# Performance work log

Measured on AMD Instinct MI355X. Metric: run time of the kernel, lower is better.

Reference implementation:

```python
import jax, jax.numpy as jnp
import numpy as np
from jax.scipy.linalg import solve_triangular

D = 1792  # feature dim, divisible by m=28
B = 8192  # batch (columns of X)


def setup_inputs() -> dict:
    key = jax.random.key(0)
    k1, k2 = jax.random.split(key)
    X = jax.random.normal(k1, (D, B), dtype=jnp.float32)
    # matches torch.zeros((d,d)).normal_(0, 0.05)
    U = jax.random.normal(k2, (D, D), dtype=jnp.float32) * 0.05
    return {"X": X, "U": U}


def reference(X, U):
    """Product of d Householder reflections applied to X.

    Original math (sequential_mult): for row = d-1..0:
        X <- X - 2 v_row (v_row^T X),  v_row = U[row] / ||U[row]||
    i.e. X <- H_0 H_1 ... H_{d-1} X with H_i = I - 2 v_i v_i^T.

    We use the compact WY representation instead of the sequential loop:
        P = H_0 ... H_{d-1} = I - W^T V_n
    where rows w_k of W satisfy w_k = 2 v_k - 2 sum_{j<k} (v_j . v_k) w_j,
    i.e. (I + 2 * strict_tril(G)) W = 2 V_n with G = V_n V_n^T.
    This is the same math, expressed with GEMMs + one triangular solve.
    """
    Vn = U / jnp.linalg.norm(U, axis=1, keepdims=True)          # (d, d) unit reflector rows
    G = Vn @ Vn.T                                               # (d, d) gram of reflectors
    T = jnp.eye(D, dtype=X.dtype) + 2.0 * jnp.tril(G, k=-1)    # unit-diag lower triangular
    Wt = solve_triangular(T, 2.0 * Vn, lower=True)              # (d, d): rows are w_k
    return X - Wt.T @ (Vn @ X)                                  # P @ X
```

## Files before the change

kernel.cpp:

```cpp
#include <hip/hip_runtime.h>
#include <stdint.h>
#include <stddef.h>

typedef _Float16 half_t;
typedef _Float16 half8 __attribute__((ext_vector_type(8)));
typedef float float4v __attribute__((ext_vector_type(4)));

#define D_DIM 1792
#define B_DIM 8192

__device__ __forceinline__ void stage_rows(const half_t* __restrict__ src, int row0, int ld,
                                           int k0, half_t* dst, int nchunks, int tid) {
  for (int base = 0; base < nchunks; base += 256) {
    int ch  = base + tid;
    int row = ch >> 2, kc = ch & 3;
    int swz = kc ^ ((row >> 1) & 3);
    const half_t* g = src + (size_t)(row0 + row) * ld + k0 + swz * 8;
    half_t* l = dst + (size_t)(base + (tid & 192)) * 8;
    __builtin_amdgcn_global_load_lds(
        (const __attribute__((address_space(1))) uint32_t*)(const void*)g,
        (__attribute__((address_space(3))) uint32_t*)(void*)l, 16, 0, 0);
  }
}

__device__ __forceinline__ void stage_rows64(const half_t* __restrict__ src, int row0, int ld,
                                             int k0, half_t* dst, int nchunks, int tid) {
  for (int base = 0; base < nchunks; base += 256) {
    int ch  = base + tid;
    int row = ch >> 3, kc = ch & 7;
    int swz = kc ^ (row & 7);
    const half_t* g = src + (size_t)(row0 + row) * ld + k0 + swz * 8;
    half_t* l = dst + (size_t)(base + (tid & 192)) * 8;
    __builtin_amdgcn_global_load_lds(
        (const __attribute__((address_space(1))) uint32_t*)(const void*)g,
        (__attribute__((address_space(3))) uint32_t*)(void*)l, 16, 0, 0);
  }
}

__device__ __forceinline__ half8 frag32(const half_t* lds, int row, int chunk) {
  int slot = chunk ^ ((row >> 1) & 3);
  return *(const half8*)(lds + row * 32 + slot * 8);
}
__device__ __forceinline__ half8 frag64(const half_t* lds, int row, int chunk) {
  int slot = chunk ^ (row & 7);
  return *(const half8*)(lds + row * 64 + slot * 8);
}

__global__ __launch_bounds__(256) void normalize_rows(const float* __restrict__ U,
                                                      half_t* __restrict__ Vh) {
  int r = blockIdx.x, t = threadIdx.x;
  float v[7];
  float s = 0.f;
#pragma unroll
  for (int i = 0; i < 7; ++i) {
    v[i] = U[(size_t)r * D_DIM + t + i * 256];
    s += v[i] * v[i];
  }
#pragma unroll
  for (int m = 32; m; m >>= 1) s += __shfl_xor(s, m);
  __shared__ float red[4];
  __shared__ float tot;
  if ((t & 63) == 0) red[t >> 6] = s;
  __syncthreads();
  if (t == 0) tot = 1.0f / sqrtf(red[0] + red[1] + red[2] + red[3]);
  __syncthreads();
  float rn = tot;
#pragma unroll
  for (int i = 0; i < 7; ++i)
    Vh[(size_t)r * D_DIM + t + i * 256] = (half_t)(v[i] * rn);
}

__global__ __launch_bounds__(256) void transpose_x(const float* __restrict__ X,
                                                   half_t* __restrict__ XT) {
  __shared__ half_t t[64][68];
  int r0 = blockIdx.x * 64, c0 = blockIdx.y * 64;
  int tid = threadIdx.x;
#pragma unroll
  for (int i = 0; i < 16; ++i) {
    int f = tid + i * 256;
    int rr = f >> 6, cc = f & 63;
    t[rr][cc] = (half_t)X[(size_t)(r0 + rr) * B_DIM + c0 + cc];
  }
  __syncthreads();
#pragma unroll
  for (int i = 0; i < 16; ++i) {
    int f = tid + i * 256;
    int cc = f >> 6, rr = f & 63;
    XT[(size_t)(c0 + cc) * D_DIM + r0 + rr] = t[rr][cc];
  }
}

__global__ __launch_bounds__(256) void transpose_h(const half_t* __restrict__ Vh,
                                                   half_t* __restrict__ VhT) {
  __shared__ half_t t[64][68];
  int r0 = blockIdx.x * 64, c0 = blockIdx.y * 64;
  int tid = threadIdx.x;
#pragma unroll
  for (int i = 0; i < 16; ++i) {
    int f = tid + i * 256;
    int rr = f >> 6, cc = f & 63;
    t[rr][cc] = Vh[(size_t)(r0 + rr) * D_DIM + c0 + cc];
  }
  __syncthreads();
#pragma unroll
  for (int i = 0; i < 16; ++i) {
    int f = tid + i * 256;
    int cc = f >> 6, rr = f & 63;
    VhT[(size_t)(c0 + cc) * D_DIM + r0 + rr] = t[rr][cc];
  }
}

__global__ __launch_bounds__(256) void zero_tri(half_t* __restrict__ Tinv,
                                                half_t* __restrict__ TinvT) {
  int bc = blockIdx.x, br = blockIdx.y;
  int tid = threadIdx.x;
  half8 z = {};
  if (bc > br) {
    for (int it = 0; it < 8; ++it) {
      int ch = it * 256 + tid;
      int r = ch >> 4, c = (ch & 15) * 8;
      *(half8*)(Tinv + (size_t)(br * 128 + r) * D_DIM + bc * 128 + c) = z;
    }
  } else if (bc < br) {
    for (int it = 0; it < 8; ++it) {
      int ch = it * 256 + tid;
      int r = ch >> 4, c = (ch & 15) * 8;
      *(half8*)(TinvT + (size_t)(br * 128 + r) * D_DIM + bc * 128 + c) = z;
    }
  }
}

template <int MODE>
__global__ __launch_bounds__(256) void gemm_nt(const half_t* __restrict__ A,
                                               const half_t* __restrict__ B,
                                               float* __restrict__ Cf, half_t* __restrict__ Ch,
                                               int K, int lda, int ldb, int ldc) {
  int bx = blockIdx.x, by = blockIdx.y;
  if constexpr (MODE == 2) {
    int id = bx + gridDim.x * by;
    int xcd = id & 7, s = id >> 3;
    by = s % 14;
    bx = (s / 14) * 8 + xcd;
  }
  int m0 = by * 128, n0 = bx * 128;
  __shared__ half_t sA0[128 * 32], sB0[128 * 32];
  __shared__ half_t sA1[128 * 32], sB1[128 * 32];
  int tid = threadIdx.x, lane = tid & 63, wave = tid >> 6;
  int ln15 = lane & 15, quad = lane >> 4;
  int wr = (wave & 1) * 64, wc = (wave >> 1) * 64;
  float4v acc[4][4] = {};
  int KB = K / 32;
  auto compute = [&](const half_t* cA, const half_t* cB) {
    half8 af[4], bf[4];
#pragma unroll
    for (int i = 0; i < 4; ++i) af[i] = frag32(cA, wr + i * 16 + ln15, quad);
#pragma unroll
    for (int j = 0; j < 4; ++j) bf[j] = frag32(cB, wc + j * 16 + ln15, quad);
#pragma unroll
    for (int i = 0; i < 4; ++i)
#pragma unroll
      for (int j = 0; j < 4; ++j)
        acc[i][j] = __builtin_amdgcn_mfma_f32_16x16x32_f16(af[i], bf[j], acc[i][j], 0, 0, 0);
  };
  stage_rows(A, m0, lda, 0, sA0, 512, tid);
  stage_rows(B, n0, ldb, 0, sB0, 512, tid);
  for (int kb = 0; kb < KB; kb += 2) {
    stage_rows(A, m0, lda, (kb + 1) * 32, sA1, 512, tid);
    stage_rows(B, n0, ldb, (kb + 1) * 32, sB1, 512, tid);
    asm volatile("s_waitcnt vmcnt(4)" ::: "memory");
    __builtin_amdgcn_s_barrier();
    __builtin_amdgcn_sched_barrier(0);
    compute(sA0, sB0);
    __builtin_amdgcn_sched_barrier(0);
    __builtin_amdgcn_s_barrier();
    if (kb + 2 < KB) {
      stage_rows(A, m0, lda, (kb + 2) * 32, sA0, 512, tid);
      stage_rows(B, n0, ldb, (kb + 2) * 32, sB0, 512, tid);
      asm volatile("s_waitcnt vmcnt(4)" ::: "memory");
    } else {
      asm volatile("s_waitcnt vmcnt(0)" ::: "memory");
    }
    __builtin_amdgcn_s_barrier();
    __builtin_amdgcn_sched_barrier(0);
    compute(sA1, sB1);
    __builtin_amdgcn_sched_barrier(0);
    __builtin_amdgcn_s_barrier();
  }
#pragma unroll
  for (int i = 0; i < 4; ++i)
#pragma unroll
    for (int j = 0; j < 4; ++j)
#pragma unroll
      for (int rg = 0; rg < 4; ++rg) {
        int row = m0 + wr + i * 16 + quad * 4 + rg;
        int col = n0 + wc + j * 16 + ln15;
        Cf[(size_t)row * ldc + col] = acc[i][j][rg];
      }
}

template <int MODE>
__global__ __launch_bounds__(256) void gemm64(const half_t* __restrict__ A,
                                              const half_t* __restrict__ B,
                                              half_t* __restrict__ Ch,
                                              int K, int lda, int ldb, int ldc) {
  int m0 = blockIdx.y * 64, n0 = blockIdx.x * 64;
  if constexpr (MODE == 0) { if (n0 > m0) return; }
  int Keff = K;
  if constexpr (MODE == 3) Keff = n0 + 64;
  __shared__ half_t sA0[64 * 32], sB0[64 * 32];
  __shared__ half_t sA1[64 * 32], sB1[64 * 32];
  int tid = threadIdx.x, lane = tid & 63, wave = tid >> 6;
  int ln15 = lane & 15, quad = lane >> 4;
  int wr = (wave & 1) * 32, wc = (wave >> 1) * 32;
  float4v acc[2][2] = {};
  int KB = Keff / 32;
  auto compute = [&](const half_t* cA, const half_t* cB) {
    half8 af[2], bf[2];
#pragma unroll
    for (int i = 0; i < 2; ++i) af[i] = frag32(cA, wr + i * 16 + ln15, quad);
#pragma unroll
    for (int j = 0; j < 2; ++j) bf[j] = frag32(cB, wc + j * 16 + ln15, quad);
#pragma unroll
    for (int i = 0; i < 2; ++i)
#pragma unroll
      for (int j = 0; j < 2; ++j)
        acc[i][j] = __builtin_amdgcn_mfma_f32_16x16x32_f16(af[i], bf[j], acc[i][j], 0, 0, 0);
  };
  stage_rows(A, m0, lda, 0, sA0, 256, tid);
  stage_rows(B, n0, ldb, 0, sB0, 256, tid);
  for (int kb = 0; kb < KB; kb += 2) {
    stage_rows(A, m0, lda, (kb + 1) * 32, sA1, 256, tid);
    stage_rows(B, n0, ldb, (kb + 1) * 32, sB1, 256, tid);
    asm volatile("s_waitcnt vmcnt(2)" ::: "memory");
    __builtin_amdgcn_s_barrier();
    __builtin_amdgcn_sched_barrier(0);
    compute(sA0, sB0);
    __builtin_amdgcn_sched_barrier(0);
    __builtin_amdgcn_s_barrier();
    if (kb + 2 < KB) {
      stage_rows(A, m0, lda, (kb + 2) * 32, sA0, 256, tid);
      stage_rows(B, n0, ldb, (kb + 2) * 32, sB0, 256, tid);
      asm volatile("s_waitcnt vmcnt(2)" ::: "memory");
    } else {
      asm volatile("s_waitcnt vmcnt(0)" ::: "memory");
    }
    __builtin_amdgcn_s_barrier();
    __builtin_amdgcn_sched_barrier(0);
    compute(sA1, sB1);
    __builtin_amdgcn_sched_barrier(0);
    __builtin_amdgcn_s_barrier();
  }
#pragma unroll
  for (int i = 0; i < 2; ++i)
#pragma unroll
    for (int j = 0; j < 2; ++j)
#pragma unroll
      for (int rg = 0; rg < 4; ++rg) {
        int row = m0 + wr + i * 16 + quad * 4 + rg;
        int col = n0 + wc + j * 16 + ln15;
        size_t idx = (size_t)row * ldc + col;
        float v = acc[i][j][rg];
        if constexpr (MODE == 0) Ch[idx] = (col < row) ? (half_t)(2.0f * v) : (half_t)0.0f;
        else if constexpr (MODE == 1) Ch[idx] = (half_t)(((row == col) ? 1.0f : 0.0f) - v);
        else Ch[idx] = (half_t)(2.0f * v);
      }
}

__global__ __launch_bounds__(256) void diag_inv(const half_t* __restrict__ T16,
                                                half_t* __restrict__ Tinv,
                                                half_t* __restrict__ TinvT) {
  int b = blockIdx.x >> 5;
  int cg = blockIdx.x & 31;
  int wave = threadIdx.x >> 6, ln = threadIdx.x & 63;
  int c = cg * 4 + wave;
  __shared__ float Ls[128][128];
  __shared__ float xw[4][128];
  for (int i = 0; i < 64; ++i) {
    int f = threadIdx.x + i * 256;
    int r = f >> 7, cc = f & 127;
    Ls[r][cc] = (cc < r) ? (float)T16[(size_t)(b * 128 + r) * D_DIM + b * 128 + cc] : 0.0f;
  }
  __syncthreads();
  float xlo = (ln == 0) ? 1.f : 0.f, xhi = 0.f;
  for (int r = c + 1; r < 128; ++r) {
    float ta = 0.f;
    int j0 = c + ln, j1 = c + 64 + ln;
    if (j0 < r) ta += Ls[r][j0] * xlo;
    if (j1 < r) ta += Ls[r][j1] * xhi;
#pragma unroll
    for (int m = 32; m; m >>= 1) ta += __shfl_xor(ta, m);
    float xr = -ta;
    if (j0 == r) xlo = xr;
    if (j1 == r) xhi = xr;
    if (ln == 0) xw[wave][r] = xr;
  }
  __syncthreads();
  for (int rr = ln; rr < 128; rr += 64) {
    float val = (rr < c) ? 0.f : ((rr == c) ? 1.f : xw[wave][rr]);
    half_t hv = (half_t)val;
    Tinv[(size_t)(b * 128 + rr) * D_DIM + b * 128 + c] = hv;
    TinvT[(size_t)(b * 128 + c) * D_DIM + b * 128 + rr] = hv;
  }
}

__global__ __launch_bounds__(256) void tinv64(const half_t* __restrict__ A, int ldA, long long strA,
                                              const half_t* __restrict__ B, int ldB, long long strB,
                                              half_t* __restrict__ O1, int ldO1, long long strO1,
                                              half_t* __restrict__ O2, int ldO2, long long strO2,
                                              int K, int neg) {
  long long z = blockIdx.z;
  A += z * strA;
  B += z * strB;
  O1 += z * strO1;
  if (O2) O2 += z * strO2;
  int m0 = blockIdx.y * 64, n0 = blockIdx.x * 64;
  __shared__ half_t sA0[64 * 64], sB0[64 * 64];
  __shared__ half_t sA1[64 * 64], sB1[64 * 64];
  int tid = threadIdx.x, lane = tid & 63, wave = tid >> 6;
  int ln15 = lane & 15, quad = lane >> 4;
  int wr = (wave & 1) * 32, wc = (wave >> 1) * 32;
  float4v acc[2][2] = {};
  int KB = K / 64;
  auto compute = [&](const half_t* cA, const half_t* cB) {
    half8 af[2], bf[2];
#pragma unroll
    for (int q = 0; q < 2; ++q) {
#pragma unroll
      for (int i = 0; i < 2; ++i) af[i] = frag64(cA, wr + i * 16 + ln15, q * 4 + quad);
#pragma unroll
      for (int j = 0; j < 2; ++j) bf[j] = frag64(cB, wc + j * 16 + ln15, q * 4 + quad);
#pragma unroll
      for (int i = 0; i < 2; ++i)
#pragma unroll
        for (int j = 0; j < 2; ++j)
          acc[i][j] = __builtin_amdgcn_mfma_f32_16x16x32_f16(af[i], bf[j], acc[i][j], 0, 0, 0);
    }
  };
  stage_rows64(A, m0, ldA, 0, sA0, 512, tid);
  stage_rows64(B, n0, ldB, 0, sB0, 512, tid);
  for (int kb = 0; kb < KB; kb += 2) {
    stage_rows64(A, m0, ldA, (kb + 1) * 64, sA1, 512, tid);
    stage_rows64(B, n0, ldB, (kb + 1) * 64, sB1, 512, tid);
    asm volatile("s_waitcnt vmcnt(4)" ::: "memory");
    __builtin_amdgcn_s_barrier();
    __builtin_amdgcn_sched_barrier(0);
    compute(sA0, sB0);
    __builtin_amdgcn_sched_barrier(0);
    __builtin_amdgcn_s_barrier();
    if (kb + 2 < KB) {
      stage_rows64(A, m0, ldA, (kb + 2) * 64, sA0, 512, tid);
      stage_rows64(B, n0, ldB, (kb + 2) * 64, sB0, 512, tid);
      asm volatile("s_waitcnt vmcnt(4)" ::: "memory");
    } else {
      asm volatile("s_waitcnt vmcnt(0)" ::: "memory");
    }
    __builtin_amdgcn_s_barrier();
    __builtin_amdgcn_sched_barrier(0);
    compute(sA1, sB1);
    __builtin_amdgcn_sched_barrier(0);
    __builtin_amdgcn_s_barrier();
  }
#pragma unroll
  for (int i = 0; i < 2; ++i)
#pragma unroll
    for (int j = 0; j < 2; ++j)
#pragma unroll
      for (int rg = 0; rg < 4; ++rg) {
        int m = m0 + wr + i * 16 + quad * 4 + rg;
        int n = n0 + wc + j * 16 + ln15;
        float v = acc[i][j][rg];
        if (neg) v = -v;
        half_t hv = (half_t)v;
        O1[(size_t)m * ldO1 + n] = hv;
        if (O2) O2[(size_t)n * ldO2 + m] = hv;
      }
}

extern "C" void kernel_launch(void* const* d_in, const int* in_sizes, int n_in,
                              void* d_out, int out_size, void* d_ws, size_t ws_size,
                              hipStream_t stream) {
  (void)in_sizes; (void)n_in; (void)out_size; (void)ws_size;
  const float* X = (const float*)d_in[0];
  const float* U = (const float*)d_in[1];
  float* out = (float*)d_out;

  char* ws = (char*)d_ws;
  half_t* Tinv  = (half_t*)(ws);
  half_t* XT    = (half_t*)(ws);
  half_t* Vh    = (half_t*)(ws + 29360128);
  half_t* scr   = Vh;
  half_t* VhT   = (half_t*)(ws + 35782656);
  half_t* T16   = (half_t*)(ws + 42205184);
  half_t* WtT   = (half_t*)(ws + 48627712);
  half_t* TinvT = (half_t*)(ws + 55050240);
  half_t* Pf    = TinvT;

  const int D = D_DIM;

  normalize_rows<<<dim3(D), dim3(256), 0, stream>>>(U, Vh);
  gemm64<0><<<dim3(28, 28), dim3(256), 0, stream>>>(Vh, Vh, T16, D, D, D, D);
  transpose_h<<<dim3(28, 28), dim3(256), 0, stream>>>(Vh, VhT);
  diag_inv<<<dim3(448), dim3(256), 0, stream>>>(T16, Tinv, TinvT);
  zero_tri<<<dim3(14, 14), dim3(256), 0, stream>>>(Tinv, TinvT);

  {
    long long st = 256LL * D + 256;
    tinv64<<<dim3(2, 2, 7), dim3(256), 0, stream>>>(
        TinvT, D, st, T16 + 128LL * D, D, st, scr, 128, 16384, nullptr, 0, 0, 128, 0);
    tinv64<<<dim3(2, 2, 7), dim3(256), 0, stream>>>(
        scr, 128, 16384, Tinv + 128LL * D + 128, D, st,
        TinvT + 128, D, st, Tinv + 128LL * D, D, st, 128, 1);
  }
  {
    long long st = 512LL * D + 512;
    tinv64<<<dim3(4, 4, 3), dim3(256), 0, stream>>>(
        TinvT, D, st, T16 + 256LL * D, D, st, scr, 256, 65536, nullptr, 0, 0, 256, 0);
    tinv64<<<dim3(4, 4, 3), dim3(256), 0, stream>>>(
        scr, 256, 65536, Tinv + 256LL * D + 256, D, st,
        TinvT + 256, D, st, Tinv + 256LL * D, D, st, 256, 1);
  }
  tinv64<<<dim3(8, 8, 1), dim3(256), 0, stream>>>(
      TinvT, D, 0, T16 + 512LL * D, D, 0, scr, 512, 0, nullptr, 0, 0, 512, 0);
  tinv64<<<dim3(8, 8, 1), dim3(256), 0, stream>>>(
      scr, 512, 0, Tinv + 512LL * D + 512, D, 0,
      TinvT + 512, D, 0, Tinv + 512LL * D, D, 0, 512, 1);
  tinv64<<<dim3(4, 8, 1), dim3(256), 0, stream>>>(
      TinvT + 1024LL * D + 1024, D, 0, T16 + 1536LL * D + 1024, D, 0,
      scr, 256, 0, nullptr, 0, 0, 512, 0);
  tinv64<<<dim3(4, 8, 1), dim3(256), 0, stream>>>(
      scr, 256, 0, Tinv + 1536LL * D + 1536, D, 0,
      TinvT + 1024LL * D + 1536, D, 0, Tinv + 1536LL * D + 1024, D, 0, 256, 1);
  tinv64<<<dim3(12, 16, 1), dim3(256), 0, stream>>>(
      TinvT, D, 0, T16 + 1024LL * D, D, 0, scr, 768, 0, nullptr, 0, 0, 1024, 0);
  tinv64<<<dim3(12, 16, 1), dim3(256), 0, stream>>>(
      scr, 768, 0, Tinv + 1024LL * D + 1024, D, 0,
      TinvT + 1024, D, 0, Tinv + 1024LL * D, D, 0, 768, 1);

  gemm64<3><<<dim3(28, 28), dim3(256), 0, stream>>>(VhT, Tinv, WtT, 0, D, D, D);
  transpose_x<<<dim3(D / 64, B_DIM / 64), dim3(256), 0, stream>>>(X, XT);
  gemm64<1><<<dim3(28, 28), dim3(256), 0, stream>>>(WtT, VhT, Pf, D, D, D, D);
  gemm_nt<2><<<dim3(64, 14), dim3(256), 0, stream>>>(Pf, XT, out, nullptr, D, D, D, B_DIM);
}
```

Measured before the change: 382.5 us.

## Use 256x256 tiles with 512 threads and K=64 stages for output GEMM

Replaces the 128x128, 256-thread output GEMM with a 256x256 tile kernel that uses 8 waves, 64-wide K slices, and a double-buffered global_load_lds pipeline across 224 blocks remapped per XCD. Larger tiles raise arithmetic intensity and reduce redundant global/L2 traffic for the dominant D x B GEMM. In exchange, LDS use rises to 128 KB per block and each wave holds 32 accumulators, which limits occupancy. With only 224 blocks, some of the 256 CUs sit idle.

```diff
diff --git a/kernel.cpp b/kernel.cpp
--- a/kernel.cpp
+++ b/kernel.cpp
@@ -37,6 +37,20 @@
   }
 }
 
+__device__ __forceinline__ void stage512(const half_t* __restrict__ src, int row0, int ld,
+                                         int k0, half_t* dst, int tid) {
+  for (int base = 0; base < 2048; base += 512) {
+    int ch  = base + tid;
+    int row = ch >> 3, kc = ch & 7;
+    int swz = kc ^ (row & 7);
+    const half_t* g = src + (size_t)(row0 + row) * ld + k0 + swz * 8;
+    half_t* l = dst + (size_t)(base + (tid & 448)) * 8;
+    __builtin_amdgcn_global_load_lds(
+        (const __attribute__((address_space(1))) uint32_t*)(const void*)g,
+        (__attribute__((address_space(3))) uint32_t*)(void*)l, 16, 0, 0);
+  }
+}
+
 __device__ __forceinline__ half8 frag32(const half_t* lds, int row, int chunk) {
   int slot = chunk ^ ((row >> 1) & 3);
   return *(const half8*)(lds + row * 32 + slot * 8);
@@ -130,71 +144,64 @@
   }
 }
 
-template <int MODE>
-__global__ __launch_bounds__(256) void gemm_nt(const half_t* __restrict__ A,
-                                               const half_t* __restrict__ B,
-                                               float* __restrict__ Cf, half_t* __restrict__ Ch,
-                                               int K, int lda, int ldb, int ldc) {
-  int bx = blockIdx.x, by = blockIdx.y;
-  if constexpr (MODE == 2) {
-    int id = bx + gridDim.x * by;
-    int xcd = id & 7, s = id >> 3;
-    by = s % 14;
-    bx = (s / 14) * 8 + xcd;
-  }
-  int m0 = by * 128, n0 = bx * 128;
-  __shared__ half_t sA0[128 * 32], sB0[128 * 32];
-  __shared__ half_t sA1[128 * 32], sB1[128 * 32];
-  int tid = threadIdx.x, lane = tid & 63, wave = tid >> 6;
+__global__ __launch_bounds__(512) void gemm_out(const half_t* __restrict__ A,
+                                                const half_t* __restrict__ B,
+                                                float* __restrict__ C,
+                                                int K, int lda, int ldb, int ldc) {
+  int id = blockIdx.x;
+  int xcd = id & 7, s = id >> 3;
+  int by = s % 7;
+  int bx = (s / 7) * 8 + xcd;
+  int m0 = by * 256, n0 = bx * 256;
+  __shared__ half_t sA[2][256 * 64];
+  __shared__ half_t sB[2][256 * 64];
+  int tid = threadIdx.x, lane = tid & 63;
+  int wv = tid >> 6, wr = wv & 1, wc = wv >> 1;
   int ln15 = lane & 15, quad = lane >> 4;
-  int wr = (wave & 1) * 64, wc = (wave >> 1) * 64;
-  float4v acc[4][4] = {};
-  int KB = K / 32;
-  auto compute = [&](const half_t* cA, const half_t* cB) {
-    half8 af[4], bf[4];
-#pragma unroll
-    for (int i = 0; i < 4; ++i) af[i] = frag32(cA, wr + i * 16 + ln15, quad);
-#pragma unroll
-    for (int j = 0; j < 4; ++j) bf[j] = frag32(cB, wc + j * 16 + ln15, quad);
-#pragma unroll
-    for (int i = 0; i < 4; ++i)
-#pragma unroll
-      for (int j = 0; j < 4; ++j)
-        acc[i][j] = __builtin_amdgcn_mfma_f32_16x16x32_f16(af[i], bf[j], acc[i][j], 0, 0, 0);
-  };
-  stage_rows(A, m0, lda, 0, sA0, 512, tid);
-  stage_rows(B, n0, ldb, 0, sB0, 512, tid);
-  for (int kb = 0; kb < KB; kb += 2) {
-    stage_rows(A, m0, lda, (kb + 1) * 32, sA1, 512, tid);
-    stage_rows(B, n0, ldb, (kb + 1) * 32, sB1, 512, tid);
-    asm volatile("s_waitcnt vmcnt(4)" ::: "memory");
-    __builtin_amdgcn_s_barrier();
-    __builtin_amdgcn_sched_barrier(0);
-    compute(sA0, sB0);
-    __builtin_amdgcn_sched_barrier(0);
-    __builtin_amdgcn_s_barrier();
-    if (kb + 2 < KB) {
-      stage_rows(A, m0, lda, (kb + 2) * 32, sA0, 512, tid);
-      stage_rows(B, n0, ldb, (kb + 2) * 32, sB0, 512, tid);
-      asm volatile("s_waitcnt vmcnt(4)" ::: "memory");
-    } else {
-      asm volatile("s_waitcnt vmcnt(0)" ::: "memory");
-    }
-    __builtin_amdgcn_s_barrier();
-    __builtin_amdgcn_sched_barrier(0);
-    compute(sA1, sB1);
-    __builtin_amdgcn_sched_barrier(0);
-    __builtin_amdgcn_s_barrier();
-  }
-#pragma unroll
-  for (int i = 0; i < 4; ++i)
+  float4v acc[8][4] = {};
+  int NT = K / 64;
+  stage512(A, m0, lda, 0, &sA[0][0], tid);
+  stage512(B, n0, ldb, 0, &sB[0][0], tid);
+  stage512(A, m0, lda, 64, &sA[1][0], tid);
+  stage512(B, n0, ldb, 64, &sB[1][0], tid);
+  for (int t = 0; t < NT; ++t) {
+    if (t + 1 < NT) asm volatile("s_waitcnt vmcnt(8)" ::: "memory");
+    else            asm volatile("s_waitcnt vmcnt(0)" ::: "memory");
+    __builtin_amdgcn_s_barrier();
+    int b = t & 1;
+    const half_t* cA = &sA[b][0];
+    const half_t* cB = &sB[b][0];
+    half8 bf[4][2];
 #pragma unroll
     for (int j = 0; j < 4; ++j)
 #pragma unroll
+      for (int q = 0; q < 2; ++q)
+        bf[j][q] = frag64(cB, wc * 64 + j * 16 + ln15, q * 4 + quad);
+#pragma unroll
+    for (int i = 0; i < 8; ++i) {
+      half8 a0 = frag64(cA, wr * 128 + i * 16 + ln15, quad);
+      half8 a1 = frag64(cA, wr * 128 + i * 16 + ln15, 4 + quad);
+#pragma unroll
+      for (int j = 0; j < 4; ++j) {
+        acc[i][j] = __builtin_amdgcn_mfma_f32_16x16x32_f16(a0, bf[j][0], acc[i][j], 0, 0, 0);
+        acc[i][j] = __builtin_amdgcn_mfma_f32_16x16x32_f16(a1, bf[j][1], acc[i][j], 0, 0, 0);
+      }
+    }
+    __builtin_amdgcn_s_barrier();
+    if (t + 2 < NT) {
+      stage512(A, m0, lda, (t + 2) * 64, &sA[b][0], tid);
+      stage512(B, n0, ldb, (t + 2) * 64, &sB[b][0], tid);
+    }
+  }
+#pragma unroll
+  for (int i = 0; i < 8; ++i)
+#pragma unroll
+    for (int j = 0; j < 4; ++j)
+#pragma unroll
       for (int rg = 0; rg < 4; ++rg) {
-        int row = m0 + wr + i * 16 + quad * 4 + rg;
-        int col = n0 + wc + j * 16 + ln15;
-        Cf[(size_t)row * ldc + col] = acc[i][j][rg];
+        int row = m0 + wr * 128 + i * 16 + quad * 4 + rg;
+        int col = n0 + wc * 64 + j * 16 + ln15;
+        C[(size_t)row * ldc + col] = acc[i][j][rg];
       }
 }
 
@@ -439,5 +446,5 @@
   gemm64<3><<<dim3(28, 28), dim3(256), 0, stream>>>(VhT, Tinv, WtT, 0, D, D, D);
   transpose_x<<<dim3(D / 64, B_DIM / 64), dim3(256), 0, stream>>>(X, XT);
   gemm64<1><<<dim3(28, 28), dim3(256), 0, stream>>>(WtT, VhT, Pf, D, D, D, D);
-  gemm_nt<2><<<dim3(64, 14), dim3(256), 0, stream>>>(Pf, XT, out, nullptr, D, D, D, B_DIM);
-}
+  gemm_out<<<dim3(224), dim3(512), 0, stream>>>(Pf, XT, out, D, D, D, B_DIM);
+}
```

Measured after the change: 363.4 us. 1.05x faster.
